# Kernel optimization log

Measured on AMD Instinct MI355X. Metric: run time of the kernel, lower is better.

## Reference

```python
import jax, jax.numpy as jnp
import numpy as np

DEL_ID, STOP_ID, PAD_ID, KEEP_ID = 3, 5, 0, 2


def lstm(x, h0, c0, Wi, Wh, bi, bh):
    """Single-layer batch-first LSTM, PyTorch gate order (i,f,g,o).
    x: [B,T,E]; h0,c0: [B,H]. Returns (ys [B,T,H], h [B,H], c [B,H])."""
    b = bi + bh

    def step(carry, xt):
        h, c = carry
        g = xt @ Wi.T + h @ Wh.T + b  # [B,4H]
        i, f, gg, o = jnp.split(g, 4, axis=-1)
        c = jax.nn.sigmoid(f) * c + jax.nn.sigmoid(i) * jnp.tanh(gg)
        h = jax.nn.sigmoid(o) * jnp.tanh(c)
        return (h, c), h

    (h, c), ys = jax.lax.scan(step, (h0, c0), jnp.swapaxes(x, 0, 1))
    return jnp.swapaxes(ys, 0, 1), h, c


def setup_inputs() -> dict:
    key = jax.random.key(0)
    ks = jax.random.split(key, 20)
    B, T, S, H, E, V = 32, 100, 100, 512, 256, 30000
    s = 0.02
    inp = {
        "input_edits": jax.random.randint(ks[0], (B, T), 0, V),
        "simp_sent": jax.random.randint(ks[1], (B, S), 0, V),
        "org_ids": jax.random.randint(ks[2], (B, S), 0, V),
        "encoder_outputs_org": jax.random.normal(ks[3], (B, S, H), dtype=jnp.float32),
        "h0": jnp.zeros((B, H), jnp.float32),
        "c0": jnp.zeros((B, H), jnp.float32),
        "emb": jax.random.normal(ks[4], (V, E), dtype=jnp.float32) * s,
        "Wi_e": jax.random.normal(ks[5], (4 * H, E), dtype=jnp.float32) * s,
        "Wh_e": jax.random.normal(ks[6], (4 * H, H), dtype=jnp.float32) * s,
        "bi_e": jnp.zeros((4 * H,), jnp.float32),
        "bh_e": jnp.zeros((4 * H,), jnp.float32),
        "Wi_w": jax.random.normal(ks[7], (4 * H, E), dtype=jnp.float32) * s,
        "Wh_w": jax.random.normal(ks[8], (4 * H, H), dtype=jnp.float32) * s,
        "bi_w": jnp.zeros((4 * H,), jnp.float32),
        "bh_w": jnp.zeros((4 * H,), jnp.float32),
        "Wp": jax.random.normal(ks[9], (H, H), dtype=jnp.float32) * s,
        "Wm": jax.random.normal(ks[10], (E, 4 * H), dtype=jnp.float32) * s,
        "bm": jnp.zeros((E,), jnp.float32),
        "b_out": jnp.zeros((30000,), jnp.float32),
    }
    return inp


def reference(input_edits, simp_sent, org_ids, encoder_outputs_org, h0, c0,
              emb, Wi_e, Wh_e, bi_e, bh_e, Wi_w, Wh_w, bi_w, bh_w,
              Wp, Wm, bm, b_out):
    # teacher_forcing_ratio = 1.0 -> teacher-forcing branch only
    B, T = input_edits.shape
    S = encoder_outputs_org.shape[1]
    Sw = simp_sent.shape[1]

    # run both LSTMs over the full teacher-forced sequences
    out_e, he, ce = lstm(emb[input_edits], h0, c0, Wi_e, Wh_e, bi_e, bh_e)  # [B,T,H]
    out_w, _, _ = lstm(emb[simp_sent], h0, c0, Wi_w, Wh_w, bi_w, bh_w)      # [B,Sw,H]

    # attention over encoder outputs
    key_org = out_e @ Wp.T                                                   # [B,T,H]
    attn = jax.nn.softmax(jnp.einsum('bth,bsh->bts', key_org, encoder_outputs_org), axis=-1)
    applied = jnp.einsum('bts,bsh->bth', attn, encoder_outputs_org)          # [B,T,H]

    # counters are exclusive cumsums of gold-action masks over input_edits[:,1:]
    a = input_edits[:, 1:]                                                   # gold actions, [B,T-1]
    inc_del = ((a == KEEP_ID) | (a == DEL_ID)).astype(jnp.int32)
    inc_ins = ((a != DEL_ID) & (a != STOP_ID) & (a != PAD_ID)).astype(jnp.int32)
    ctr_del = jnp.clip(jnp.cumsum(inc_del, 1) - inc_del, 0, S - 1)           # [B,T-1]
    ctr_ins = jnp.clip(jnp.cumsum(inc_ins, 1) - inc_ins, 0, Sw - 1)

    H = encoder_outputs_org.shape[2]
    c = jnp.take_along_axis(encoder_outputs_org,
                            jnp.broadcast_to(ctr_del[:, :, None], (B, T - 1, H)), axis=1)
    c_word = jnp.take_along_axis(out_w,
                                 jnp.broadcast_to(ctr_ins[:, :, None], (B, T - 1, H)), axis=1)

    feat = jnp.concatenate([out_e[:, :T - 1], applied[:, :T - 1], c, c_word], axis=-1)  # [B,T-1,4H]
    hmlp = jnp.tanh(feat @ Wm.T + bm)                                        # [B,T-1,E]
    logp = jax.nn.log_softmax(hmlp @ emb.T + b_out, axis=-1)                 # [B,T-1,V]
    return logp, he[None], ce[None]
```

## Files before the change

kernel.cpp:

```cpp
#include <hip/hip_runtime.h>
#include <math.h>


typedef __attribute__((ext_vector_type(8))) short short8v;
typedef __attribute__((ext_vector_type(4))) float f32x4;
typedef unsigned long long ull;

#define LSTM_BLOCKS 64
#define NTIL 235

__device__ __forceinline__ float sigf(float x){ return 1.0f/(1.0f + __expf(-x)); }
__device__ __forceinline__ float tanhc(float x){
  x = fminf(fmaxf(x, -15.f), 15.f);
  float e = __expf(2.f*x);
  return (e-1.f)/(e+1.f);
}
__device__ __forceinline__ short f2bf(float f){
  unsigned u = __float_as_uint(f);
  u = (u + 0x7fffu + ((u >> 16) & 1u)) >> 16;
  return (short)u;
}
__device__ __forceinline__ float bf2f(short s){
  return __uint_as_float(((unsigned)(unsigned short)s) << 16);
}

__global__ void prep_permute(
    const float* __restrict__ Wi_e, const float* __restrict__ Wh_e,
    const float* __restrict__ bi_e, const float* __restrict__ bh_e,
    const float* __restrict__ Wi_w, const float* __restrict__ Wh_w,
    const float* __restrict__ bi_w, const float* __restrict__ bh_w,
    short* __restrict__ WiPh_e, short* __restrict__ WhPh_e, float* __restrict__ biasP_e,
    short* __restrict__ WiPh_w, short* __restrict__ WhPh_w, float* __restrict__ biasP_w)
{
  const int z = blockIdx.y;
  const float* Wi = z ? Wi_w : Wi_e;
  const float* Wh = z ? Wh_w : Wh_e;
  const float* bi = z ? bi_w : bi_e;
  const float* bh = z ? bh_w : bh_e;
  short* WiPh = z ? WiPh_w : WiPh_e;
  short* WhPh = z ? WhPh_w : WhPh_e;
  float* biasP = z ? biasP_w : biasP_e;

  int idx = blockIdx.x*256 + threadIdx.x;
  {
    int op = idx >> 9, k = idx & 511;
    int u = op >> 2, g = op & 3;
    WhPh[idx] = f2bf(Wh[(g*512+u)*512 + k]);
  }
  if (idx < 2048*256) {
    int op = idx >> 8, e = idx & 255;
    int u = op >> 2, g = op & 3;
    WiPh[idx] = f2bf(Wi[(g*512+u)*256 + e]);
  }
  if (idx < 2048) {
    int u = idx >> 2, g = idx & 3;
    biasP[idx] = bi[g*512+u] + bh[g*512+u];
  }
}

__global__ void misc_prep(const float* __restrict__ emb,
                          const float* __restrict__ Wp, const float* __restrict__ Wm,
                          const float* __restrict__ h0, const int* __restrict__ ie,
                          short* __restrict__ embh,
                          short* __restrict__ Wph, short* __restrict__ Wmh,
                          ull* __restrict__ hq, unsigned* __restrict__ flags,
                          int* __restrict__ ctr_del, int* __restrict__ ctr_ins)
{
  int idx = blockIdx.x*256 + threadIdx.x;
  if (idx < 1920000) {
    float4 v = *(const float4*)(emb + (long)idx*4);
    short4 o; o.x=f2bf(v.x); o.y=f2bf(v.y); o.z=f2bf(v.z); o.w=f2bf(v.w);
    *(short4*)(embh + (long)idx*4) = o;
  } else if (idx < 1985536) {
    int i = idx - 1920000;
    float4 v = *(const float4*)(Wp + (long)i*4);
    short4 o; o.x=f2bf(v.x); o.y=f2bf(v.y); o.z=f2bf(v.z); o.w=f2bf(v.w);
    *(short4*)(Wph + (long)i*4) = o;
  } else if (idx < 2116608) {
    int i = idx - 1985536;
    float4 v = *(const float4*)(Wm + (long)i*4);
    short4 o; o.x=f2bf(v.x); o.y=f2bf(v.y); o.z=f2bf(v.z); o.w=f2bf(v.w);
    *(short4*)(Wmh + (long)i*4) = o;
  } else if (idx < 2124800) {
    int i = idx - 2116608;
    int b = (i >> 7) & 31, q = i & 127;
    const float* src = h0 + b*512 + q*4;
    ull v = ((ull)(unsigned short)f2bf(src[3]) << 48) |
            ((ull)(unsigned short)f2bf(src[2]) << 32) |
            ((ull)(unsigned short)f2bf(src[1]) << 16) |
            ((ull)(unsigned short)f2bf(src[0]));
    hq[i] = v;
  } else if (idx < 2124928) {
    flags[idx - 2124800] = 0u;
  } else if (idx < 2124960) {
    int b = idx - 2124928;
    int rd = 0, ri = 0;
    for (int t = 0; t < 99; ++t) {
      int a = ie[b*100 + t + 1];
      int incd = (a == 2 || a == 3) ? 1 : 0;
      int inci = (a != 3 && a != 5 && a != 0) ? 1 : 0;
      ctr_del[b*99 + t] = min(rd, 99);
      ctr_ins[b*99 + t] = min(ri, 99);
      rd += incd; ri += inci;
    }
  }
}

__global__ __launch_bounds__(256) void enc_prep(const float* __restrict__ enc,
                                                short* __restrict__ ench,
                                                short* __restrict__ encTh)
{
  __shared__ short tile[100][72];
  const int b = blockIdx.x;
  const float* src = enc + (long)b*51200;
  short* de = ench  + (long)b*51200;
  short* dt = encTh + (long)b*65536;
  const int tid = threadIdx.x;
  for (int c = 0; c < 8; ++c) {
    #pragma unroll
    for (int i = 0; i < 25; ++i) {
      int idx = tid + 256*i;
      int k = idx >> 6, j = idx & 63;
      short h = f2bf(src[(long)k*512 + c*64 + j]);
      tile[k][j] = h;
      de[(long)k*512 + c*64 + j] = h;
    }
    __syncthreads();
    #pragma unroll
    for (int i = 0; i < 32; ++i) {
      int idx = tid + 256*i;
      int n = idx >> 7, kk = idx & 127;
      dt[(long)(c*64 + n)*128 + kk] = (kk < 100) ? tile[kk][n] : (short)0;
    }
    __syncthreads();
  }
}

template<int GATHER,int CVT_A,int BIAS,int TANH,int OUT_BF16,int HQ>
__device__ __forceinline__ void gemm_mfma_body(
    const void* __restrict__ Av, const int* __restrict__ tok,
    const short* __restrict__ Bh, const float* __restrict__ bias,
    void* __restrict__ Cv, int M, int N, int K, int lda, int ldc,
    int bxk, int byk)
{
  __shared__ short As[128][72];
  __shared__ short Bs[128][72];
  const int bm = bxk * 128;
  const int bn = byk * 128;
  const int tid = threadIdx.x;
  const int w = tid >> 6, l = tid & 63;
  const int wr = (w >> 1) * 64, wc = (w & 1) * 64;
  const int lr = l & 15, kg = l >> 4;

  f32x4 acc[4][4] = {};

  for (int k0 = 0; k0 < K; k0 += 64) {
    #pragma unroll
    for (int q = 0; q < 4; ++q) {
      int ci = tid + 256*q;
      int r = ci >> 3, ch = ci & 7;
      int ar = bm + r; if (ar > M-1) ar = M-1;
      if (GATHER) ar = tok[ar];
      if (CVT_A) {
        const float* ap = ((const float*)Av) + (long)ar*lda + k0 + ch*8;
        float4 v0 = *(const float4*)ap;
        float4 v1 = *(const float4*)(ap + 4);
        short8v s;
        s[0]=f2bf(v0.x); s[1]=f2bf(v0.y); s[2]=f2bf(v0.z); s[3]=f2bf(v0.w);
        s[4]=f2bf(v1.x); s[5]=f2bf(v1.y); s[6]=f2bf(v1.z); s[7]=f2bf(v1.w);
        *(short8v*)&As[r][ch*8] = s;
      } else if (HQ) {
        int bb = ar / 100, tt = ar % 100;
        const short* ap = ((const short*)Av) + (long)(tt+1)*32768
                        + (long)lda*16384 + bb*512 + k0 + ch*8;
        *(short8v*)&As[r][ch*8] = *(const short8v*)ap;
      } else {
        *(short8v*)&As[r][ch*8] =
            *(const short8v*)(((const short*)Av) + (long)ar*lda + k0 + ch*8);
      }
      int br = bn + r; if (br > N-1) br = N-1;
      *(short8v*)&Bs[r][ch*8] = *(const short8v*)(Bh + (long)br*K + k0 + ch*8);
    }
    __syncthreads();
    #pragma unroll
    for (int ks = 0; ks < 2; ++ks) {
      short8v a[4], b[4];
      #pragma unroll
      for (int m = 0; m < 4; ++m)
        a[m] = *(const short8v*)&As[wr + m*16 + lr][ks*32 + kg*8];
      #pragma unroll
      for (int n = 0; n < 4; ++n)
        b[n] = *(const short8v*)&Bs[wc + n*16 + lr][ks*32 + kg*8];
      #pragma unroll
      for (int m = 0; m < 4; ++m)
        #pragma unroll
        for (int n = 0; n < 4; ++n)
          acc[m][n] = __builtin_amdgcn_mfma_f32_16x16x32_bf16(a[m], b[n], acc[m][n], 0, 0, 0);
    }
    __syncthreads();
  }

  #pragma unroll
  for (int n = 0; n < 4; ++n) {
    int col = bn + wc + n*16 + lr;
    bool cok = (col < N);
    float bv = (BIAS && cok) ? bias[col] : 0.f;
    #pragma unroll
    for (int m = 0; m < 4; ++m) {
      int row0 = bm + wr + m*16 + kg*4;
      #pragma unroll
      for (int r = 0; r < 4; ++r) {
        int row = row0 + r;
        if (cok && row < M) {
          float v = acc[m][n][r] + bv;
          if (TANH) v = tanhc(v);
          if (OUT_BF16) ((short*)Cv)[(long)row*ldc + col] = f2bf(v);
          else          ((float*)Cv)[(long)row*ldc + col] = v;
        }
      }
    }
  }
}

template<int GATHER,int CVT_A,int BIAS,int TANH,int OUT_BF16,int HQ>
__global__ __launch_bounds__(256) void gemm_mfma(
    const void* __restrict__ Av, const int* __restrict__ tok,
    const short* __restrict__ Bh, const float* __restrict__ bias,
    void* __restrict__ Cv, int M, int N, int K, int lda, int ldc)
{
  gemm_mfma_body<GATHER,CVT_A,BIAS,TANH,OUT_BF16,HQ>(
      Av, tok, Bh, bias, Cv, M, N, K, lda, ldc, blockIdx.x, blockIdx.y);
}

template<int BIAS,int TANH,int OUT_BF16>
__global__ __launch_bounds__(256) void gemm_mfma_bat(
    const short* __restrict__ Ah, const short* __restrict__ Bh,
    const float* __restrict__ bias, void* __restrict__ Cv,
    int M, int N, int K, int lda, int ldc, long sA, long sB, long sC)
{
  const int z = blockIdx.z;
  void* C2 = OUT_BF16 ? (void*)((short*)Cv + (long)z*sC)
                      : (void*)((float*)Cv + (long)z*sC);
  gemm_mfma_body<0,0,BIAS,TANH,OUT_BF16,0>(
      (const void*)(Ah + (long)z*sA), nullptr, Bh + (long)z*sB, bias,
      C2, M, N, K, lda, ldc, blockIdx.x, blockIdx.y);
}

__global__ __launch_bounds__(256) void xproj_mfma(
    const float* __restrict__ emb,
    const int* __restrict__ tokA, const int* __restrict__ tokB,
    const short* __restrict__ WA, const short* __restrict__ WB,
    const float* __restrict__ bA, const float* __restrict__ bB,
    short* __restrict__ outA, short* __restrict__ outB)
{
  const int z = blockIdx.z;
  gemm_mfma_body<1,1,1,0,1,0>(
      emb, z ? tokB : tokA, z ? WB : WA, z ? bB : bA,
      z ? (void*)outB : (void*)outA, 3200, 2048, 256, 256, 2048,
      blockIdx.x, blockIdx.y);
}

__global__ __launch_bounds__(256) void logits_mfma_partial(
    const short* __restrict__ Ah,
    const short* __restrict__ Bh,
    const float* __restrict__ bias,
    short* __restrict__ Cg,
    float2* __restrict__ partial)
{
  __shared__ short As[128][72];
  __shared__ short Bs[128][72];
  __shared__ float2 red[128][2];
  const int bm = blockIdx.x * 128;
  const int bn = blockIdx.y * 128;
  const int tid = threadIdx.x;
  const int w = tid >> 6, l = tid & 63;
  const int wr = (w >> 1) * 64, wc = (w & 1) * 64;
  const int lr = l & 15, kg = l >> 4;

  f32x4 acc[4][4] = {};

  #pragma unroll
  for (int k0 = 0; k0 < 256; k0 += 64) {
    #pragma unroll
    for (int q = 0; q < 4; ++q) {
      int ci = tid + 256*q;
      int r = ci >> 3, ch = ci & 7;
      int ar = bm + r; if (ar > 3167) ar = 3167;
      *(short8v*)&As[r][ch*8] = *(const short8v*)(Ah + (long)ar*256 + k0 + ch*8);
      int br = bn + r; if (br > 29999) br = 29999;
      *(short8v*)&Bs[r][ch*8] = *(const short8v*)(Bh + (long)br*256 + k0 + ch*8);
    }
    __syncthreads();
    #pragma unroll
    for (int ks = 0; ks < 2; ++ks) {
      short8v a[4], b[4];
      #pragma unroll
      for (int m = 0; m < 4; ++m)
        a[m] = *(const short8v*)&As[wr + m*16 + lr][ks*32 + kg*8];
      #pragma unroll
      for (int n = 0; n < 4; ++n)
        b[n] = *(const short8v*)&Bs[wc + n*16 + lr][ks*32 + kg*8];
      #pragma unroll
      for (int m = 0; m < 4; ++m)
        #pragma unroll
        for (int n = 0; n < 4; ++n)
          acc[m][n] = __builtin_amdgcn_mfma_f32_16x16x32_bf16(a[m], b[n], acc[m][n], 0, 0, 0);
    }
    __syncthreads();
  }

  #pragma unroll
  for (int n = 0; n < 4; ++n) {
    int col = bn + wc + n*16 + lr;
    float bv = (col < 30000) ? bias[col] : 0.f;
    #pragma unroll
    for (int m = 0; m < 4; ++m)
      #pragma unroll
      for (int r = 0; r < 4; ++r)
        acc[m][n][r] = (col < 30000) ? acc[m][n][r] + bv : -INFINITY;
  }
  #pragma unroll
  for (int m = 0; m < 4; ++m) {
    #pragma unroll
    for (int r = 0; r < 4; ++r) {
      float a0 = acc[m][0][r], a1 = acc[m][1][r], a2 = acc[m][2][r], a3 = acc[m][3][r];
      float mx = fmaxf(fmaxf(a0, a1), fmaxf(a2, a3));
      #pragma unroll
      for (int off = 1; off < 16; off <<= 1) mx = fmaxf(mx, __shfl_xor(mx, off));
      float se = 0.f;
      if (mx > -INFINITY)
        se = __expf(a0-mx) + __expf(a1-mx) + __expf(a2-mx) + __expf(a3-mx);
      #pragma unroll
      for (int off = 1; off < 16; off <<= 1) se += __shfl_xor(se, off);
      if (lr == 0) red[wr + m*16 + kg*4 + r][w & 1] = make_float2(mx, se);
    }
  }
  #pragma unroll
  for (int n = 0; n < 4; ++n) {
    int col = bn + wc + n*16 + lr;
    if (col < 30000) {
      #pragma unroll
      for (int m = 0; m < 4; ++m) {
        int row0 = bm + wr + m*16 + kg*4;
        #pragma unroll
        for (int r = 0; r < 4; ++r) {
          int row = row0 + r;
          if (row < 3168) Cg[(long)row*30000 + col] = f2bf(acc[m][n][r]);
        }
      }
    }
  }
  __syncthreads();
  if (tid < 128) {
    int row = bm + tid;
    if (row < 3168) {
      float2 A = red[tid][0], B = red[tid][1];
      float M = fmaxf(A.x, B.x);
      float S = 0.f;
      if (M > -INFINITY) S = A.y*__expf(A.x - M) + B.y*__expf(B.x - M);
      partial[(long)row*NTIL + blockIdx.y] = make_float2(M, S);
    }
  }
}

__global__ __launch_bounds__(256) void sub_lse_fused(
    const short* __restrict__ Cg, const float2* __restrict__ partial,
    float* __restrict__ out)
{
  int row = blockIdx.x;
  int tid = threadIdx.x;
  float m = -INFINITY, s = 0.f;
  if (tid < NTIL) {
    float2 p = partial[(long)row*NTIL + tid];
    m = p.x; s = p.y;
  }
  #pragma unroll
  for (int off = 32; off; off >>= 1) {
    float om = __shfl_xor(m, off);
    float os = __shfl_xor(s, off);
    float nm = fmaxf(m, om);
    if (nm > -INFINITY) {
      s = s*__expf(m - nm) + os*__expf(om - nm);
      m = nm;
    }
  }
  __shared__ float sm[4], ss[4], lsh;
  int wv = tid >> 6;
  if ((tid & 63) == 0) { sm[wv] = m; ss[wv] = s; }
  __syncthreads();
  if (tid == 0) {
    float M = sm[0], S = ss[0];
    #pragma unroll
    for (int i = 1; i < 4; ++i) {
      float nm = fmaxf(M, sm[i]);
      S = S*__expf(M - nm) + ss[i]*__expf(sm[i] - nm);
      M = nm;
    }
    lsh = M + __logf(S);
  }
  __syncthreads();
  float lv = lsh;
  const short* src = Cg + (long)row*30000;
  float* dst = out + (long)row*30000;
  for (int i = tid; i < 3750; i += 256) {
    short8v v = *(const short8v*)(src + i*8);
    float4 o0, o1;
    o0.x = bf2f(v[0]) - lv; o0.y = bf2f(v[1]) - lv;
    o0.z = bf2f(v[2]) - lv; o0.w = bf2f(v[3]) - lv;
    o1.x = bf2f(v[4]) - lv; o1.y = bf2f(v[5]) - lv;
    o1.z = bf2f(v[6]) - lv; o1.w = bf2f(v[7]) - lv;
    *(float4*)(dst + i*8)     = o0;
    *(float4*)(dst + i*8 + 4) = o1;
  }
}

__global__ __launch_bounds__(256, 1) void lstm_persist(
    const short* __restrict__ WhPh_e, const short* __restrict__ WhPh_w,
    const short* __restrict__ Xp_e, const short* __restrict__ Xp_w,
    const float* __restrict__ c0_in,
    ull* __restrict__ hq,
    float* __restrict__ out_hc,
    unsigned* __restrict__ flags)
{
  const int bx = blockIdx.x;
  const int l = bx >> 5;
  const int ublk = bx & 31;
  const int tid = threadIdx.x;
  const int w = tid >> 6, lane = tid & 63;
  const int uloc = lane >> 4;
  const int bn = lane & 15;
  const int u_global = ublk*16 + w*4 + uloc;
  const int ob = (ublk*16 + w*4) * 4;
  const int qcol = ublk*4 + w;

  const short* WhPh = l ? WhPh_w : WhPh_e;
  const short* Xp   = l ? Xp_w   : Xp_e;
  const unsigned* myfl = flags + l*32;

  __shared__ short hT[32][520];

  __hip_atomic_load(&flags[100], __ATOMIC_ACQUIRE, __HIP_MEMORY_SCOPE_AGENT);

  short8v afr[16];
  {
    const short* wp = WhPh + (long)(ob + bn)*512 + uloc*8;
    #pragma unroll
    for (int ks = 0; ks < 16; ++ks)
      afr[ks] = *(const short8v*)(wp + ks*32);
  }
  float c_s0 = c0_in[bn*512 + u_global];
  float c_s1 = c0_in[(bn+16)*512 + u_global];

  for (int t = 0; t < 100; ++t) {
    ull xq0 = *(const ull*)(Xp + ((long)(bn*100 + t))*2048 + u_global*4);
    ull xq1 = *(const ull*)(Xp + ((long)((bn+16)*100 + t))*2048 + u_global*4);
    if (t) {
      int ok;
      do {
        unsigned f = (lane < 32)
          ? __hip_atomic_load(&myfl[lane], __ATOMIC_RELAXED, __HIP_MEMORY_SCOPE_AGENT)
          : 0xffffffffu;
        ok = __all((int)(f >= (unsigned)t));
        if (!ok) __builtin_amdgcn_s_sleep(1);
      } while (!ok);
    }
    {
      const ull* hsrc = hq + (size_t)t*8192 + (l << 12);
      #pragma unroll
      for (int i = 0; i < 16; ++i) {
        int idx = tid + 256*i;
        int b = idx >> 7, q = idx & 127;
        *(ull*)&hT[b][q*4] = hsrc[idx];
      }
    }
    __syncthreads();
    f32x4 acc0 = {}, acc1 = {};
    #pragma unroll
    for (int ks = 0; ks < 16; ++ks) {
      short8v b0 = *(const short8v*)&hT[bn][ks*32 + uloc*8];
      short8v b1 = *(const short8v*)&hT[bn+16][ks*32 + uloc*8];
      acc0 = __builtin_amdgcn_mfma_f32_16x16x32_bf16(afr[ks], b0, acc0, 0, 0, 0);
      acc1 = __builtin_amdgcn_mfma_f32_16x16x32_bf16(afr[ks], b1, acc1, 0, 0, 0);
    }
    float gi = acc0[0] + bf2f((short)(xq0 & 0xffffu));
    float gf = acc0[1] + bf2f((short)((xq0 >> 16) & 0xffffu));
    float gg = acc0[2] + bf2f((short)((xq0 >> 32) & 0xffffu));
    float go = acc0[3] + bf2f((short)((xq0 >> 48) & 0xffffu));
    c_s0 = sigf(gf)*c_s0 + sigf(gi)*tanhc(gg);
    float hv0 = sigf(go)*tanhc(c_s0);
    gi = acc1[0] + bf2f((short)(xq1 & 0xffffu));
    gf = acc1[1] + bf2f((short)((xq1 >> 16) & 0xffffu));
    gg = acc1[2] + bf2f((short)((xq1 >> 32) & 0xffffu));
    go = acc1[3] + bf2f((short)((xq1 >> 48) & 0xffffu));
    c_s1 = sigf(gf)*c_s1 + sigf(gi)*tanhc(gg);
    float hv1 = sigf(go)*tanhc(c_s1);

    short hb0 = f2bf(hv0), hb1 = f2bf(hv1);
    unsigned p0 = (unsigned)(unsigned short)hb0;
    unsigned p1 = (unsigned)(unsigned short)hb1;
    unsigned a1 = __shfl_down((int)p0, 16), a2 = __shfl_down((int)p0, 32), a3 = __shfl_down((int)p0, 48);
    unsigned e1 = __shfl_down((int)p1, 16), e2 = __shfl_down((int)p1, 32), e3 = __shfl_down((int)p1, 48);
    if (uloc == 0) {
      ull q0 = ((ull)((a2 & 0xffffu) | (a3 << 16)) << 32) | ((p0 & 0xffffu) | (a1 << 16));
      ull q1 = ((ull)((e2 & 0xffffu) | (e3 << 16)) << 32) | ((p1 & 0xffffu) | (e1 << 16));
      ull* hd = hq + (size_t)(t+1)*8192 + (l << 12);
      __hip_atomic_store(&hd[(bn << 7) + qcol],      q0, __ATOMIC_RELAXED, __HIP_MEMORY_SCOPE_AGENT);
      __hip_atomic_store(&hd[((bn+16) << 7) + qcol], q1, __ATOMIC_RELAXED, __HIP_MEMORY_SCOPE_AGENT);
    }
    if (t < 99) {
      asm volatile("s_waitcnt vmcnt(0)" ::: "memory");
      __syncthreads();
      if (tid == 0)
        __hip_atomic_store(&flags[bx], (unsigned)(t+1),
                           __ATOMIC_RELAXED, __HIP_MEMORY_SCOPE_AGENT);
    }
    if (t == 99 && l == 0) {
      out_hc[bn*512 + u_global]              = hv0;
      out_hc[(bn+16)*512 + u_global]         = hv1;
      out_hc[16384 + bn*512 + u_global]      = c_s0;
      out_hc[16384 + (bn+16)*512 + u_global] = c_s1;
    }
  }
}

__global__ void softmax_rows(const float* __restrict__ P, short* __restrict__ Ph)
{
  int row  = blockIdx.x*4 + (threadIdx.x >> 6);
  int lane = threadIdx.x & 63;
  const float* p = P + (long)row*128;
  short* q = Ph + (long)row*128;
  float x0 = p[lane];
  float x1 = (lane + 64 < 100) ? p[lane+64] : -INFINITY;
  float m = fmaxf(x0, x1);
  #pragma unroll
  for (int off = 32; off; off >>= 1) m = fmaxf(m, __shfl_xor(m, off));
  float e0 = __expf(x0 - m);
  float e1 = (lane + 64 < 100) ? __expf(x1 - m) : 0.f;
  float s = e0 + e1;
  #pragma unroll
  for (int off = 32; off; off >>= 1) s += __shfl_xor(s, off);
  float inv = 1.f / s;
  q[lane]      = f2bf(e0 * inv);
  q[lane + 64] = (lane + 64 < 100) ? f2bf(e1 * inv) : (short)0;
}

__global__ void feat_kernel(const short* __restrict__ hqs, const short* __restrict__ appliedh,
                            const short* __restrict__ ench,
                            const int* __restrict__ ctr_del, const int* __restrict__ ctr_ins,
                            short* __restrict__ feat)
{
  int n = blockIdx.x;
  int b = n / 99, t = n % 99;
  int tid = threadIdx.x;
  int seg = tid >> 6;
  int off = (tid & 63) * 8;
  const short* s = (seg == 0) ? hqs + (long)(t+1)*32768 + b*512
                 : (seg == 1) ? appliedh + (long)(b*100 + t)*512
                 : (seg == 2) ? ench + (long)(b*100 + ctr_del[n])*512
                              : hqs + (long)(ctr_ins[n]+1)*32768 + 16384 + b*512;
  *(short8v*)(feat + (long)n*2048 + seg*512 + off) = *(const short8v*)(s + off);
}

extern "C" void kernel_launch(void* const* d_in, const int* in_sizes, int n_in,
                              void* d_out, int out_size, void* d_ws, size_t ws_size,
                              hipStream_t stream)
{
  const int*   input_edits = (const int*)  d_in[0];
  const int*   simp_sent   = (const int*)  d_in[1];
  const float* enc   = (const float*)d_in[3];
  const float* h0    = (const float*)d_in[4];
  const float* c0    = (const float*)d_in[5];
  const float* emb   = (const float*)d_in[6];
  const float* Wi_e  = (const float*)d_in[7];
  const float* Wh_e  = (const float*)d_in[8];
  const float* bi_e  = (const float*)d_in[9];
  const float* bh_e  = (const float*)d_in[10];
  const float* Wi_w  = (const float*)d_in[11];
  const float* Wh_w  = (const float*)d_in[12];
  const float* bi_w  = (const float*)d_in[13];
  const float* bh_w  = (const float*)d_in[14];
  const float* Wp    = (const float*)d_in[15];
  const float* Wm    = (const float*)d_in[16];
  const float* bmv   = (const float*)d_in[17];
  const float* b_out = (const float*)d_in[18];
  float* out = (float*)d_out;

  float* ws = (float*)d_ws;
  size_t off = 0;
  auto alloc = [&](size_t n){ float* p = ws + off; off += (n + 63) & ~(size_t)63; return p; };

  short* WiPh_e   = (short*)alloc(262144);
  short* WiPh_w   = (short*)alloc(262144);
  float* biasP_e  = alloc(2048);
  float* biasP_w  = alloc(2048);
  short* WhPh_e   = (short*)alloc(524288);
  short* WhPh_w   = (short*)alloc(524288);
  short* Xp_e     = (short*)alloc(3276800);
  short* Xp_w     = (short*)alloc(3276800);
  ull*   hq       = (ull*)alloc(101*8192*2);
  unsigned* flags = (unsigned*)alloc(128);
  float* Pbuf     = alloc(409600);
  short* Pbh      = (short*)alloc(204800);
  int*   ctr_del  = (int*)alloc(3168);
  int*   ctr_ins  = (int*)alloc(3168);
  short* Wph      = (short*)alloc(131072);
  short* Wmh      = (short*)alloc(262144);
  short* keyh     = (short*)alloc(819200);
  short* appliedh = (short*)alloc(819200);
  short* ench     = (short*)alloc(819200);
  short* encTh    = (short*)alloc(1048576);
  short* embh     = (short*)alloc(3840000);
  short* logith   = (short*)alloc(47520000);
  float2* partial = (float2*)alloc(3168*NTIL*2);
  short* feath    = (short*)Xp_e;
  short* hmlph    = (short*)Xp_w;

  prep_permute<<<dim3(4096,2), 256, 0, stream>>>(
      Wi_e, Wh_e, bi_e, bh_e, Wi_w, Wh_w, bi_w, bh_w,
      WiPh_e, WhPh_e, biasP_e, WiPh_w, WhPh_w, biasP_w);
  misc_prep<<<8301, 256, 0, stream>>>(emb, Wp, Wm, h0, input_edits,
                                      embh, Wph, Wmh, hq, flags, ctr_del, ctr_ins);
  enc_prep<<<32, 256, 0, stream>>>(enc, ench, encTh);

  xproj_mfma<<<dim3(25,16,2), 256, 0, stream>>>(
      emb, input_edits, simp_sent, WiPh_e, WiPh_w, biasP_e, biasP_w, Xp_e, Xp_w);

  lstm_persist<<<LSTM_BLOCKS, 256, 0, stream>>>(
      WhPh_e, WhPh_w, Xp_e, Xp_w, c0, hq, out + 95040000L, flags);

  gemm_mfma<0,0,0,0,1,1><<<dim3(25,4), 256, 0, stream>>>(
      hq, nullptr, Wph, nullptr, keyh, 3200, 512, 512, 0 , 512);

  gemm_mfma_bat<0,0,0><<<dim3(1,1,32), 256, 0, stream>>>(
      keyh, ench, nullptr, Pbuf, 100, 100, 512, 512, 128,
      51200, 51200, 12800);
  softmax_rows<<<800, 256, 0, stream>>>(Pbuf, Pbh);
  gemm_mfma_bat<0,0,1><<<dim3(1,4,32), 256, 0, stream>>>(
      Pbh, encTh, nullptr, appliedh, 100, 512, 128, 128, 512,
      12800, 65536, 51200);

  feat_kernel<<<3168, 256, 0, stream>>>((const short*)hq, appliedh, ench,
                                        ctr_del, ctr_ins, feath);
  gemm_mfma<0,0,1,1,1,0><<<dim3(25,2), 256, 0, stream>>>(
      feath, nullptr, Wmh, bmv, hmlph, 3168, 256, 2048, 2048, 256);

  logits_mfma_partial<<<dim3(25, NTIL), 256, 0, stream>>>(
      hmlph, embh, b_out, logith, partial);
  sub_lse_fused<<<3168, 256, 0, stream>>>(logith, partial, out);
}
```

Baseline: 1.053 ms.

## Store LSTM hidden state in MFMA-fragment layout and read it directly from global memory

The global hidden-state buffer hq is rearranged into a tiled layout that matches the MFMA B-operand fragment order. Each lane of the persistent LSTM kernel can then load its h fragments straight from global (L2) memory, which removes the shared-memory staging copy and one __syncthreads per timestep. Producers, the init code, the HQ-gather GEMM path and feat_kernel all switch to the new indexing. In exchange, every wave issues its own global loads for the full h vector instead of sharing one staged copy.

```diff
diff --git a/kernel.cpp b/kernel.cpp
--- a/kernel.cpp
+++ b/kernel.cpp
@@ -22,6 +22,11 @@
 }
 __device__ __forceinline__ float bf2f(short s){
   return __uint_as_float(((unsigned)(unsigned short)s) << 16);
+}
+
+__device__ __forceinline__ long hq_elem(int t, int l, int b, int u0){
+  return (long)(t+1)*32768 + (long)l*16384
+       + (u0 >> 5)*1024 + (b >> 4)*512 + ((u0 >> 3) & 3)*128 + (b & 15)*8;
 }
 
 __global__ void prep_permute(
@@ -83,13 +88,15 @@
     *(short4*)(Wmh + (long)i*4) = o;
   } else if (idx < 2124800) {
     int i = idx - 2116608;
-    int b = (i >> 7) & 31, q = i & 127;
+    int l = i >> 12, rem = i & 4095;
+    int b = rem >> 7, q = rem & 127;
     const float* src = h0 + b*512 + q*4;
     ull v = ((ull)(unsigned short)f2bf(src[3]) << 48) |
             ((ull)(unsigned short)f2bf(src[2]) << 32) |
             ((ull)(unsigned short)f2bf(src[1]) << 16) |
             ((ull)(unsigned short)f2bf(src[0]));
-    hq[i] = v;
+    int pos = (q >> 3)*256 + (b >> 4)*128 + ((q >> 1) & 3)*32 + (b & 15)*2 + (q & 1);
+    hq[(l << 12) + pos] = v;
   } else if (idx < 2124928) {
     flags[idx - 2124800] = 0u;
   } else if (idx < 2124960) {
@@ -171,8 +178,7 @@
         *(short8v*)&As[r][ch*8] = s;
       } else if (HQ) {
         int bb = ar / 100, tt = ar % 100;
-        const short* ap = ((const short*)Av) + (long)(tt+1)*32768
-                        + (long)lda*16384 + bb*512 + k0 + ch*8;
+        const short* ap = ((const short*)Av) + hq_elem(tt, lda, bb, k0 + ch*8);
         *(short8v*)&As[r][ch*8] = *(const short8v*)ap;
       } else {
         *(short8v*)&As[r][ch*8] =
@@ -431,14 +437,11 @@
   const int bn = lane & 15;
   const int u_global = ublk*16 + w*4 + uloc;
   const int ob = (ublk*16 + w*4) * 4;
-  const int qcol = ublk*4 + w;
 
   const short* WhPh = l ? WhPh_w : WhPh_e;
   const short* Xp   = l ? Xp_w   : Xp_e;
   const unsigned* myfl = flags + l*32;
 
-  __shared__ short hT[32][520];
-
   __hip_atomic_load(&flags[100], __ATOMIC_ACQUIRE, __HIP_MEMORY_SCOPE_AGENT);
 
   short8v afr[16];
@@ -450,6 +453,9 @@
   }
   float c_s0 = c0_in[bn*512 + u_global];
   float c_s1 = c0_in[(bn+16)*512 + u_global];
+
+  const int so = ((ublk >> 1) << 8) + (((((ublk & 1) << 1) | (w >> 1))) << 5)
+               + (bn << 1) + (w & 1);
 
   for (int t = 0; t < 100; ++t) {
     ull xq0 = *(const ull*)(Xp + ((long)(bn*100 + t))*2048 + u_global*4);
@@ -464,21 +470,13 @@
         if (!ok) __builtin_amdgcn_s_sleep(1);
       } while (!ok);
     }
-    {
-      const ull* hsrc = hq + (size_t)t*8192 + (l << 12);
-      #pragma unroll
-      for (int i = 0; i < 16; ++i) {
-        int idx = tid + 256*i;
-        int b = idx >> 7, q = idx & 127;
-        *(ull*)&hT[b][q*4] = hsrc[idx];
-      }
-    }
-    __syncthreads();
+    const ull* hb = hq + (size_t)t*8192 + (l << 12);
+    const ull* r  = hb + (uloc << 5) + (bn << 1);
     f32x4 acc0 = {}, acc1 = {};
     #pragma unroll
     for (int ks = 0; ks < 16; ++ks) {
-      short8v b0 = *(const short8v*)&hT[bn][ks*32 + uloc*8];
-      short8v b1 = *(const short8v*)&hT[bn+16][ks*32 + uloc*8];
+      short8v b0 = *(const short8v*)(r + ks*256);
+      short8v b1 = *(const short8v*)(r + ks*256 + 128);
       acc0 = __builtin_amdgcn_mfma_f32_16x16x32_bf16(afr[ks], b0, acc0, 0, 0, 0);
       acc1 = __builtin_amdgcn_mfma_f32_16x16x32_bf16(afr[ks], b1, acc1, 0, 0, 0);
     }
@@ -504,8 +502,8 @@
       ull q0 = ((ull)((a2 & 0xffffu) | (a3 << 16)) << 32) | ((p0 & 0xffffu) | (a1 << 16));
       ull q1 = ((ull)((e2 & 0xffffu) | (e3 << 16)) << 32) | ((p1 & 0xffffu) | (e1 << 16));
       ull* hd = hq + (size_t)(t+1)*8192 + (l << 12);
-      __hip_atomic_store(&hd[(bn << 7) + qcol],      q0, __ATOMIC_RELAXED, __HIP_MEMORY_SCOPE_AGENT);
-      __hip_atomic_store(&hd[((bn+16) << 7) + qcol], q1, __ATOMIC_RELAXED, __HIP_MEMORY_SCOPE_AGENT);
+      __hip_atomic_store(&hd[so],       q0, __ATOMIC_RELAXED, __HIP_MEMORY_SCOPE_AGENT);
+      __hip_atomic_store(&hd[so + 128], q1, __ATOMIC_RELAXED, __HIP_MEMORY_SCOPE_AGENT);
     }
     if (t < 99) {
       asm volatile("s_waitcnt vmcnt(0)" ::: "memory");
@@ -554,11 +552,12 @@
   int tid = threadIdx.x;
   int seg = tid >> 6;
   int off = (tid & 63) * 8;
-  const short* s = (seg == 0) ? hqs + (long)(t+1)*32768 + b*512
-                 : (seg == 1) ? appliedh + (long)(b*100 + t)*512
-                 : (seg == 2) ? ench + (long)(b*100 + ctr_del[n])*512
-                              : hqs + (long)(ctr_ins[n]+1)*32768 + 16384 + b*512;
-  *(short8v*)(feat + (long)n*2048 + seg*512 + off) = *(const short8v*)(s + off);
+  const short* s;
+  if (seg == 0)      s = hqs + hq_elem(t, 0, b, off);
+  else if (seg == 1) s = appliedh + (long)(b*100 + t)*512 + off;
+  else if (seg == 2) s = ench + (long)(b*100 + ctr_del[n])*512 + off;
+  else               s = hqs + hq_elem(ctr_ins[n], 1, b, off);
+  *(short8v*)(feat + (long)n*2048 + seg*512 + off) = *(const short8v*)s;
 }
 
 extern "C" void kernel_launch(void* const* d_in, const int* in_sizes, int n_in,
```

Result: slower. 1.229 ms (+16.8%).
